# Performance work log

Measured on AMD Instinct MI355X. Metric: run time of the kernel, lower is better.

Reference implementation:

```python
import jax, jax.numpy as jnp
import numpy as np

DIM = 512
NUM_HEADS = 8
NUM_BLOCKS = 16
# NOTE: original code computes head_dim from FULL dim (before the reduce layer),
# so scale = (dim // num_heads) ** -0.5 = 64 ** -0.5, even though the actual
# per-head dim after reduce is 32. We preserve this quirk faithfully.
SCALE = (DIM // NUM_HEADS) ** -0.5


def setup_inputs() -> dict:
    key = jax.random.key(0)
    ks = jax.random.split(key, 5)
    B, N = 4, 4096
    C = DIM // 2
    x = jax.random.normal(ks[0], (B, N, DIM), dtype=jnp.float32)
    reduce_w = jax.random.normal(ks[1], (DIM, C), dtype=jnp.float32) * (DIM ** -0.5)
    qkv_w = jax.random.normal(ks[2], (C, 3 * C), dtype=jnp.float32) * (C ** -0.5)
    proj_w = jax.random.normal(ks[3], (C, DIM), dtype=jnp.float32) * (C ** -0.5)
    proj_b = jnp.zeros((DIM,), dtype=jnp.float32)
    return {"x": x, "reduce_w": reduce_w, "qkv_w": qkv_w,
            "proj_w": proj_w, "proj_b": proj_b}


def reference(x, reduce_w, qkv_w, proj_w, proj_b):
    B, N, _ = x.shape
    xr = x @ reduce_w                      # [B, N, C]  (C = dim/2)
    C = xr.shape[-1]
    H = NUM_HEADS
    d = C // H
    qkv = (xr @ qkv_w).reshape(B, N, 3, H, d).transpose(2, 0, 3, 1, 4)  # [3,B,H,N,d]
    q, k, v = qkv[0], qkv[1], qkv[2]
    bs = N // NUM_BLOCKS                   # block (chunk) size
    # block-diagonal local attention: reshape seq into independent blocks
    qb = q.reshape(B, H, NUM_BLOCKS, bs, d)
    kb = k.reshape(B, H, NUM_BLOCKS, bs, d)
    vb = v.reshape(B, H, NUM_BLOCKS, bs, d)
    attn = jnp.einsum('bhnqd,bhnkd->bhnqk', qb, kb) * SCALE
    attn = jax.nn.softmax(attn, axis=-1)
    ob = jnp.einsum('bhnqk,bhnkd->bhnqd', attn, vb)   # [B,H,Nb,bs,d]
    # torch: per-block transpose(1,2) then cat on dim=1 -> [B, N, H, d]
    o = ob.transpose(0, 2, 3, 1, 4).reshape(B, N, C)
    return o @ proj_w + proj_b
```

## Files before the change

kernel.cpp:

```cpp
#include <hip/hip_runtime.h>
#include <hip/hip_fp16.h>

typedef _Float16 half_t;
typedef _Float16 f16x8 __attribute__((ext_vector_type(8)));
typedef __fp16 fp16x2 __attribute__((ext_vector_type(2)));
typedef float f32x4 __attribute__((ext_vector_type(4)));

#define MFMA_F16(a, b, c) __builtin_amdgcn_mfma_f32_16x16x32_f16((a), (b), (c), 0, 0, 0)

static __device__ inline unsigned pkrtz(float a, float b) {
    union { fp16x2 h; unsigned u; } c;
    c.h = __builtin_amdgcn_cvt_pkrtz(a, b);
    return c.u;
}

__global__ __launch_bounds__(256) void prep(
    const float* __restrict__ qw, const float* __restrict__ rw,
    const float* __restrict__ pw, half_t* __restrict__ pw_t,
    half_t* __restrict__ Wt) {
    __shared__ __align__(16) char smem[24576];
    const int bid = blockIdx.x, tid = threadIdx.x;

    if (bid < 48) {
        char* As = smem;
        char* Bs = smem + 8192;
        const int M0 = (bid % 12) * 64, N0 = (bid / 12) * 128;
        const int lane = tid & 63, w = tid >> 6;
        const int l15 = lane & 15, l4 = lane >> 4;
        const int wrow = (w >> 1) * 32, wcol = (w & 1) * 64;
        const int pa = (l15 & 7) << 4;

        f32x4 acc[2][4];
#pragma unroll
        for (int i = 0; i < 2; ++i)
#pragma unroll
            for (int j = 0; j < 4; ++j) acc[i][j] = (f32x4){0.f, 0.f, 0.f, 0.f};

        for (int kc = 0; kc < 4; ++kc) {
            int c0 = kc * 64;
            __syncthreads();
#pragma unroll
            for (int i = 0; i < 2; ++i) {
                int j = tid + i * 256;
                int row = j >> 3, e8 = (j & 7) * 8;
                float s = (M0 + row) < 256 ? 0.18033688f : 1.f;
                f16x8 v;
#pragma unroll
                for (int e = 0; e < 8; ++e)
                    v[e] = (half_t)(qw[(size_t)(c0 + e8 + e) * 768 + M0 + row] * s);
                *(f16x8*)(As + row * 128 + ((e8 * 2) ^ ((row & 7) << 4))) = v;
            }
#pragma unroll
            for (int i = 0; i < 4; ++i) {
                int j = tid + i * 256;
                int row = j >> 3, e8 = (j & 7) * 8;
                const float* p = rw + (size_t)(N0 + row) * 256 + c0 + e8;
                float4 u0 = *(const float4*)p;
                float4 u1 = *(const float4*)(p + 4);
                f16x8 v;
                v[0] = (half_t)u0.x; v[1] = (half_t)u0.y;
                v[2] = (half_t)u0.z; v[3] = (half_t)u0.w;
                v[4] = (half_t)u1.x; v[5] = (half_t)u1.y;
                v[6] = (half_t)u1.z; v[7] = (half_t)u1.w;
                *(f16x8*)(Bs + row * 128 + ((e8 * 2) ^ ((row & 7) << 4))) = v;
            }
            __syncthreads();
#pragma unroll
            for (int ki = 0; ki < 2; ++ki) {
                f16x8 af[2], bf[4];
#pragma unroll
                for (int mi = 0; mi < 2; ++mi) {
                    int row = wrow + mi * 16 + l15;
                    af[mi] = *(const f16x8*)(As + row * 128 + (((ki * 4 + l4) << 4) ^ pa));
                }
#pragma unroll
                for (int nj = 0; nj < 4; ++nj) {
                    int row = wcol + nj * 16 + l15;
                    bf[nj] = *(const f16x8*)(Bs + row * 128 + (((ki * 4 + l4) << 4) ^ pa));
                }
#pragma unroll
                for (int mi = 0; mi < 2; ++mi)
#pragma unroll
                    for (int nj = 0; nj < 4; ++nj)
                        acc[mi][nj] = MFMA_F16(af[mi], bf[nj], acc[mi][nj]);
            }
        }
#pragma unroll
        for (int mi = 0; mi < 2; ++mi)
#pragma unroll
            for (int nj = 0; nj < 4; ++nj)
#pragma unroll
                for (int reg = 0; reg < 4; ++reg) {
                    int grow = M0 + wrow + mi * 16 + l4 * 4 + reg;
                    int gcol = N0 + wcol + nj * 16 + l15;
                    Wt[(size_t)grow * 512 + gcol] = (half_t)acc[mi][nj][reg];
                }
        return;
    }

    half_t* tile = (half_t*)smem;
    int t = bid - 48;
    int R0 = (t >> 3) * 64, C0 = (t & 7) * 64;
#pragma unroll
    for (int e = 0; e < 16; ++e) {
        int idx = tid + e * 256;
        int r = idx >> 6, c = idx & 63;
        tile[r * 72 + c] = (half_t)pw[(size_t)(R0 + r) * 512 + C0 + c];
    }
    __syncthreads();
#pragma unroll
    for (int e = 0; e < 16; ++e) {
        int idx = tid + e * 256;
        int c = idx >> 6, r = idx & 63;
        pw_t[(size_t)(C0 + c) * 256 + R0 + r] = tile[r * 72 + c];
    }
}

template <int EPI, bool AFP32, int NB, int K>
__global__ __launch_bounds__(256) void gemm_f16(
    const void* __restrict__ Aop, const half_t* __restrict__ Bt,
    void* __restrict__ Dst, const float* __restrict__ bias) {
    constexpr int nkt = K >> 6;
    constexpr int NBC = NB / 32;
    __shared__ __align__(16) char smem[8192 + NB * 128];
    char* As = smem;
    char* Bs = smem + 8192;

    const int tid = threadIdx.x;
    const int lane = tid & 63, w = tid >> 6;
    const int l15 = lane & 15, l4 = lane >> 4;
    const int wrow = (w >> 1) * 32, wcol = (w & 1) * (NB / 2);
    const int bm0 = blockIdx.x * 64;
    const int bn0 = blockIdx.y * NB;
    const int pa = (l15 & 7) << 4;

    f32x4 acc[2][NBC];
#pragma unroll
    for (int i = 0; i < 2; ++i)
#pragma unroll
        for (int j = 0; j < NBC; ++j) acc[i][j] = (f32x4){0.f, 0.f, 0.f, 0.f};

    f16x8 aReg[2], bReg[NBC];

    auto load_tile = [&](int kt) {
#pragma unroll
        for (int i = 0; i < 2; ++i) {
            int c = tid + i * 256;
            int row = c >> 3, k0 = (c & 7) * 8;
            int gk = kt * 64 + k0;
            if (AFP32) {
                const float* Af = (const float*)Aop + (size_t)(bm0 + row) * K + gk;
                float4 u0 = *(const float4*)Af;
                float4 u1 = *(const float4*)(Af + 4);
                f16x8 v;
                v[0] = (half_t)u0.x; v[1] = (half_t)u0.y;
                v[2] = (half_t)u0.z; v[3] = (half_t)u0.w;
                v[4] = (half_t)u1.x; v[5] = (half_t)u1.y;
                v[6] = (half_t)u1.z; v[7] = (half_t)u1.w;
                aReg[i] = v;
            } else {
                aReg[i] = *(const f16x8*)((const half_t*)Aop + (size_t)(bm0 + row) * K + gk);
            }
        }
#pragma unroll
        for (int i = 0; i < NBC; ++i) {
            int c = tid + i * 256;
            int row = c >> 3, k0 = (c & 7) * 8;
            bReg[i] = *(const f16x8*)(Bt + (size_t)(bn0 + row) * K + kt * 64 + k0);
        }
    };

    load_tile(0);
    for (int kt = 0; kt < nkt; ++kt) {
        __syncthreads();
#pragma unroll
        for (int i = 0; i < 2; ++i) {
            int c = tid + i * 256;
            int row = c >> 3, k0 = (c & 7) * 8;
            *(f16x8*)(As + row * 128 + ((k0 * 2) ^ ((row & 7) << 4))) = aReg[i];
        }
#pragma unroll
        for (int i = 0; i < NBC; ++i) {
            int c = tid + i * 256;
            int row = c >> 3, k0 = (c & 7) * 8;
            *(f16x8*)(Bs + row * 128 + ((k0 * 2) ^ ((row & 7) << 4))) = bReg[i];
        }
        __syncthreads();
        if (kt + 1 < nkt) load_tile(kt + 1);
#pragma unroll
        for (int ki = 0; ki < 2; ++ki) {
            f16x8 af[2], bf[NBC];
#pragma unroll
            for (int mi = 0; mi < 2; ++mi) {
                int row = wrow + mi * 16 + l15;
                af[mi] = *(const f16x8*)(As + row * 128 + (((ki * 4 + l4) << 4) ^ pa));
            }
#pragma unroll
            for (int nj = 0; nj < NBC; ++nj) {
                int row = wcol + nj * 16 + l15;
                bf[nj] = *(const f16x8*)(Bs + row * 128 + (((ki * 4 + l4) << 4) ^ pa));
            }
#pragma unroll
            for (int mi = 0; mi < 2; ++mi)
#pragma unroll
                for (int nj = 0; nj < NBC; ++nj)
                    acc[mi][nj] = MFMA_F16(af[mi], bf[nj], acc[mi][nj]);
        }
    }

#pragma unroll
    for (int mi = 0; mi < 2; ++mi) {
#pragma unroll
        for (int nj = 0; nj < NBC; ++nj) {
#pragma unroll
            for (int reg = 0; reg < 4; ++reg) {
                int grow = bm0 + wrow + mi * 16 + l4 * 4 + reg;
                int gcol = bn0 + wcol + nj * 16 + l15;
                float val = acc[mi][nj][reg];
                if (EPI == 1) {
                    int t = gcol >> 8, h = (gcol >> 5) & 7, dd = gcol & 31;
                    int b = grow >> 12, n = grow & 4095;
                    int blk = n >> 8, r = n & 255;
                    size_t base = (size_t)t * 4194304 +
                                  (size_t)((((b << 3) + h) << 4) + blk) * 8192;
                    size_t idx = (t == 2) ? base + (size_t)dd * 256 + r
                                          : base + (size_t)r * 32 + dd;
                    ((half_t*)Dst)[idx] = (half_t)val;
                } else {
                    ((float*)Dst)[(size_t)grow * 512 + gcol] = val + bias[gcol];
                }
            }
        }
    }
}

__global__ __launch_bounds__(512, 4) void attn_f16(const half_t* __restrict__ qkv_ws,
                                                   half_t* __restrict__ o_ws) {
    const int blkid = blockIdx.x;
    const int b = blkid >> 7, h = (blkid >> 4) & 7, blk = blkid & 15;
    const half_t* Q  = qkv_ws + (size_t)blkid * 8192;
    const half_t* Kp = qkv_ws + 4194304 + (size_t)blkid * 8192;
    const half_t* VT = qkv_ws + 8388608 + (size_t)blkid * 8192;

    const int tid = threadIdx.x, lane = tid & 63, w = tid >> 6;
    const int l15 = lane & 15, l4 = lane >> 4;
    const int qb = w * 32;

    f16x8 aq[2];
    aq[0] = *(const f16x8*)(Q + (qb + l15) * 32 + l4 * 8);
    aq[1] = *(const f16x8*)(Q + (qb + 16 + l15) * 32 + l4 * 8);

    float s_run[2] = {0.f, 0.f};
    f32x4 acc_o[2][2];
#pragma unroll
    for (int qg = 0; qg < 2; ++qg)
#pragma unroll
        for (int fo = 0; fo < 2; ++fo) acc_o[qg][fo] = (f32x4){0.f, 0.f, 0.f, 0.f};
    const f32x4 zero4 = (f32x4){0.f, 0.f, 0.f, 0.f};

    for (int kt = 0; kt < 4; ++kt) {
        f16x8 ka[4];
#pragma unroll
        for (int t = 0; t < 4; ++t)
            ka[t] = *(const f16x8*)(Kp + (kt * 64 + t * 16 + l15) * 32 + l4 * 8);
        f16x8 bv[2][2];
#pragma unroll
        for (int c = 0; c < 2; ++c)
#pragma unroll
            for (int fo = 0; fo < 2; ++fo)
                bv[c][fo] = *(const f16x8*)(VT + (fo * 16 + l15) * 256 + kt * 64 + c * 32 + l4 * 8);

        f32x4 st[2][4];
        __builtin_amdgcn_s_setprio(1);
#pragma unroll
        for (int qg = 0; qg < 2; ++qg)
#pragma unroll
            for (int t = 0; t < 4; ++t) st[qg][t] = MFMA_F16(ka[t], aq[qg], zero4);
        __builtin_amdgcn_s_setprio(0);

#pragma unroll
        for (int qg = 0; qg < 2; ++qg) {
            float p[4][4];
            float ps = 0.f;
#pragma unroll
            for (int t = 0; t < 4; ++t)
#pragma unroll
                for (int r = 0; r < 4; ++r) {
                    float e = exp2f(st[qg][t][r]);
                    p[t][r] = e;
                    ps += e;
                }
            ps += __shfl_xor(ps, 16);
            ps += __shfl_xor(ps, 32);
            s_run[qg] += ps;

#pragma unroll
            for (int c = 0; c < 2; ++c) {
                unsigned pk0[2], pk1[2];
#pragma unroll
                for (int rp = 0; rp < 2; ++rp) {
                    pk0[rp] = pkrtz(p[2 * c][2 * rp], p[2 * c][2 * rp + 1]);
                    pk1[rp] = pkrtz(p[2 * c + 1][2 * rp], p[2 * c + 1][2 * rp + 1]);
                }
                union { unsigned u[4]; f16x8 v; } au;
#pragma unroll
                for (int j = 0; j < 4; ++j) {
                    int src = l15 + ((((l4 & 1) << 1) + (j >> 1)) << 4);
                    unsigned g0 = (unsigned)__shfl((int)pk0[j & 1], src);
                    unsigned g1 = (unsigned)__shfl((int)pk1[j & 1], src);
                    au.u[j] = (l4 < 2) ? g0 : g1;
                }
                __builtin_amdgcn_s_setprio(1);
#pragma unroll
                for (int fo = 0; fo < 2; ++fo)
                    acc_o[qg][fo] = MFMA_F16(au.v, bv[c][fo], acc_o[qg][fo]);
                __builtin_amdgcn_s_setprio(0);
            }
        }
    }

#pragma unroll
    for (int qg = 0; qg < 2; ++qg) {
        float inv = 1.f / s_run[qg];
        float sinv[4];
#pragma unroll
        for (int r = 0; r < 4; ++r) sinv[r] = __shfl(inv, (l4 << 2) | r);
#pragma unroll
        for (int fo = 0; fo < 2; ++fo)
#pragma unroll
            for (int r = 0; r < 4; ++r) {
                int grow = b * 4096 + blk * 256 + qb + qg * 16 + l4 * 4 + r;
                o_ws[(size_t)grow * 256 + h * 32 + fo * 16 + l15] =
                    (half_t)(acc_o[qg][fo][r] * sinv[r]);
            }
    }
}

extern "C" void kernel_launch(void* const* d_in, const int* in_sizes, int n_in,
                              void* d_out, int out_size, void* d_ws, size_t ws_size,
                              hipStream_t stream) {
    const float* x        = (const float*)d_in[0];
    const float* reduce_w = (const float*)d_in[1];
    const float* qkv_w    = (const float*)d_in[2];
    const float* proj_w   = (const float*)d_in[3];
    const float* proj_b   = (const float*)d_in[4];
    char* ws = (char*)d_ws;

    half_t* qkv_ws = (half_t*)ws;
    half_t* o_buf  = (half_t*)(ws + 25165824);
    half_t* pw_t   = (half_t*)(ws + 33554432);
    half_t* Wt     = (half_t*)(ws + 33816576);

    prep<<<80, 256, 0, stream>>>(qkv_w, reduce_w, proj_w, pw_t, Wt);
    gemm_f16<1, true, 192, 512><<<dim3(256, 4), 256, 0, stream>>>(x, Wt, qkv_ws, nullptr);
    attn_f16<<<512, 512, 0, stream>>>(qkv_ws, o_buf);
    gemm_f16<2, false, 256, 256><<<dim3(256, 2), 256, 0, stream>>>(o_buf, pw_t, d_out, proj_b);
}
```

Baseline: 71.69 us.

## Fuse QKV projection into attention kernel and widen proj GEMM tiles

Result: faster. 65.04 us (-9.3%).

```diff
diff --git a/kernel.cpp b/kernel.cpp
--- a/kernel.cpp
+++ b/kernel.cpp
@@ -17,7 +17,7 @@
 __global__ __launch_bounds__(256) void prep(
     const float* __restrict__ qw, const float* __restrict__ rw,
     const float* __restrict__ pw, half_t* __restrict__ pw_t,
-    half_t* __restrict__ Wt) {
+    half_t* __restrict__ W3) {
     __shared__ __align__(16) char smem[24576];
     const int bid = blockIdx.x, tid = threadIdx.x;
 
@@ -91,9 +91,11 @@
             for (int nj = 0; nj < 4; ++nj)
 #pragma unroll
                 for (int reg = 0; reg < 4; ++reg) {
-                    int grow = M0 + wrow + mi * 16 + l4 * 4 + reg;
+                    int n = M0 + wrow + mi * 16 + l4 * 4 + reg;
                     int gcol = N0 + wcol + nj * 16 + l15;
-                    Wt[(size_t)grow * 512 + gcol] = (half_t)acc[mi][nj][reg];
+                    int part = n >> 8, hh = (n & 255) >> 5, dd = n & 31;
+                    W3[(size_t)(hh * 96 + part * 32 + dd) * 512 + gcol] =
+                        (half_t)acc[mi][nj][reg];
                 }
         return;
     }
@@ -116,139 +118,115 @@
     }
 }
 
-template <int EPI, bool AFP32, int NB, int K>
-__global__ __launch_bounds__(256) void gemm_f16(
-    const void* __restrict__ Aop, const half_t* __restrict__ Bt,
-    void* __restrict__ Dst, const float* __restrict__ bias) {
-    constexpr int nkt = K >> 6;
-    constexpr int NBC = NB / 32;
-    __shared__ __align__(16) char smem[8192 + NB * 128];
+__global__ __launch_bounds__(512, 4) void qkv_attn(
+    const float* __restrict__ X, const half_t* __restrict__ W3,
+    half_t* __restrict__ o_ws) {
+    __shared__ __align__(16) char smem[50176];
     char* As = smem;
-    char* Bs = smem + 8192;
-
-    const int tid = threadIdx.x;
-    const int lane = tid & 63, w = tid >> 6;
-    const int l15 = lane & 15, l4 = lane >> 4;
-    const int wrow = (w >> 1) * 32, wcol = (w & 1) * (NB / 2);
-    const int bm0 = blockIdx.x * 64;
-    const int bn0 = blockIdx.y * NB;
-    const int pa = (l15 & 7) << 4;
-
-    f32x4 acc[2][NBC];
-#pragma unroll
-    for (int i = 0; i < 2; ++i)
-#pragma unroll
-        for (int j = 0; j < NBC; ++j) acc[i][j] = (f32x4){0.f, 0.f, 0.f, 0.f};
-
-    f16x8 aReg[2], bReg[NBC];
-
-    auto load_tile = [&](int kt) {
-#pragma unroll
-        for (int i = 0; i < 2; ++i) {
-            int c = tid + i * 256;
-            int row = c >> 3, k0 = (c & 7) * 8;
-            int gk = kt * 64 + k0;
-            if (AFP32) {
-                const float* Af = (const float*)Aop + (size_t)(bm0 + row) * K + gk;
-                float4 u0 = *(const float4*)Af;
-                float4 u1 = *(const float4*)(Af + 4);
-                f16x8 v;
-                v[0] = (half_t)u0.x; v[1] = (half_t)u0.y;
-                v[2] = (half_t)u0.z; v[3] = (half_t)u0.w;
-                v[4] = (half_t)u1.x; v[5] = (half_t)u1.y;
-                v[6] = (half_t)u1.z; v[7] = (half_t)u1.w;
-                aReg[i] = v;
-            } else {
-                aReg[i] = *(const f16x8*)((const half_t*)Aop + (size_t)(bm0 + row) * K + gk);
-            }
-        }
-#pragma unroll
-        for (int i = 0; i < NBC; ++i) {
-            int c = tid + i * 256;
-            int row = c >> 3, k0 = (c & 7) * 8;
-            bReg[i] = *(const f16x8*)(Bt + (size_t)(bn0 + row) * K + kt * 64 + k0);
-        }
-    };
-
-    load_tile(0);
-    for (int kt = 0; kt < nkt; ++kt) {
-        __syncthreads();
-#pragma unroll
-        for (int i = 0; i < 2; ++i) {
-            int c = tid + i * 256;
-            int row = c >> 3, k0 = (c & 7) * 8;
-            *(f16x8*)(As + row * 128 + ((k0 * 2) ^ ((row & 7) << 4))) = aReg[i];
-        }
-#pragma unroll
-        for (int i = 0; i < NBC; ++i) {
-            int c = tid + i * 256;
-            int row = c >> 3, k0 = (c & 7) * 8;
-            *(f16x8*)(Bs + row * 128 + ((k0 * 2) ^ ((row & 7) << 4))) = bReg[i];
-        }
-        __syncthreads();
-        if (kt + 1 < nkt) load_tile(kt + 1);
-#pragma unroll
-        for (int ki = 0; ki < 2; ++ki) {
-            f16x8 af[2], bf[NBC];
-#pragma unroll
-            for (int mi = 0; mi < 2; ++mi) {
-                int row = wrow + mi * 16 + l15;
-                af[mi] = *(const f16x8*)(As + row * 128 + (((ki * 4 + l4) << 4) ^ pa));
-            }
-#pragma unroll
-            for (int nj = 0; nj < NBC; ++nj) {
-                int row = wcol + nj * 16 + l15;
-                bf[nj] = *(const f16x8*)(Bs + row * 128 + (((ki * 4 + l4) << 4) ^ pa));
-            }
-#pragma unroll
-            for (int mi = 0; mi < 2; ++mi)
-#pragma unroll
-                for (int nj = 0; nj < NBC; ++nj)
-                    acc[mi][nj] = MFMA_F16(af[mi], bf[nj], acc[mi][nj]);
-        }
-    }
-
-#pragma unroll
-    for (int mi = 0; mi < 2; ++mi) {
-#pragma unroll
-        for (int nj = 0; nj < NBC; ++nj) {
-#pragma unroll
-            for (int reg = 0; reg < 4; ++reg) {
-                int grow = bm0 + wrow + mi * 16 + l4 * 4 + reg;
-                int gcol = bn0 + wcol + nj * 16 + l15;
-                float val = acc[mi][nj][reg];
-                if (EPI == 1) {
-                    int t = gcol >> 8, h = (gcol >> 5) & 7, dd = gcol & 31;
-                    int b = grow >> 12, n = grow & 4095;
-                    int blk = n >> 8, r = n & 255;
-                    size_t base = (size_t)t * 4194304 +
-                                  (size_t)((((b << 3) + h) << 4) + blk) * 8192;
-                    size_t idx = (t == 2) ? base + (size_t)dd * 256 + r
-                                          : base + (size_t)r * 32 + dd;
-                    ((half_t*)Dst)[idx] = (half_t)val;
-                } else {
-                    ((float*)Dst)[(size_t)grow * 512 + gcol] = val + bias[gcol];
-                }
-            }
-        }
-    }
-}
-
-__global__ __launch_bounds__(512, 4) void attn_f16(const half_t* __restrict__ qkv_ws,
-                                                   half_t* __restrict__ o_ws) {
-    const int blkid = blockIdx.x;
-    const int b = blkid >> 7, h = (blkid >> 4) & 7, blk = blkid & 15;
-    const half_t* Q  = qkv_ws + (size_t)blkid * 8192;
-    const half_t* Kp = qkv_ws + 4194304 + (size_t)blkid * 8192;
-    const half_t* VT = qkv_ws + 8388608 + (size_t)blkid * 8192;
-
+    char* Bs = smem + 32768;
+    half_t* q_lds = (half_t*)smem;
+    half_t* k_lds = (half_t*)(smem + 16384);
+    half_t* vT    = (half_t*)(smem + 32768);
+
+    const int bid = blockIdx.x;
+    const int h = bid >> 6, gb = bid & 63, b = gb >> 4, blk = gb & 15;
     const int tid = threadIdx.x, lane = tid & 63, w = tid >> 6;
     const int l15 = lane & 15, l4 = lane >> 4;
+    const int pa = (l15 & 7) << 4;
+
+    const float* Xt = X + (size_t)(b * 4096 + blk * 256) * 512;
+    const half_t* Bh = W3 + (size_t)h * 96 * 512;
+
+    f32x4 acc[2][6];
+#pragma unroll
+    for (int i = 0; i < 2; ++i)
+#pragma unroll
+        for (int j = 0; j < 6; ++j) acc[i][j] = (f32x4){0.f, 0.f, 0.f, 0.f};
+
+    f16x8 aReg[4], bReg[2];
+
+    auto load_tile = [&](int kt) {
+#pragma unroll
+        for (int i = 0; i < 4; ++i) {
+            int J = tid + i * 512;
+            int row = J >> 3, c = (J & 7) ^ (row & 7);
+            const float* p = Xt + (size_t)row * 512 + kt * 64 + c * 8;
+            float4 u0 = *(const float4*)p;
+            float4 u1 = *(const float4*)(p + 4);
+            f16x8 v;
+            v[0] = (half_t)u0.x; v[1] = (half_t)u0.y;
+            v[2] = (half_t)u0.z; v[3] = (half_t)u0.w;
+            v[4] = (half_t)u1.x; v[5] = (half_t)u1.y;
+            v[6] = (half_t)u1.z; v[7] = (half_t)u1.w;
+            aReg[i] = v;
+        }
+        {
+            int J = tid;
+            int row = J >> 3, c = (J & 7) ^ (row & 7);
+            bReg[0] = *(const f16x8*)(Bh + (size_t)row * 512 + kt * 64 + c * 8);
+        }
+        if (tid < 256) {
+            int J = 512 + tid;
+            int row = J >> 3, c = (J & 7) ^ (row & 7);
+            bReg[1] = *(const f16x8*)(Bh + (size_t)row * 512 + kt * 64 + c * 8);
+        }
+    };
+
+    load_tile(0);
+    for (int kt = 0; kt < 8; ++kt) {
+        __syncthreads();
+#pragma unroll
+        for (int i = 0; i < 4; ++i) {
+            int J = tid + i * 512;
+            *(f16x8*)(As + J * 16) = aReg[i];
+        }
+        *(f16x8*)(Bs + tid * 16) = bReg[0];
+        if (tid < 256) *(f16x8*)(Bs + (512 + tid) * 16) = bReg[1];
+        __syncthreads();
+        if (kt + 1 < 8) load_tile(kt + 1);
+#pragma unroll
+        for (int ki = 0; ki < 2; ++ki) {
+            f16x8 af[2], bf[6];
+#pragma unroll
+            for (int mi = 0; mi < 2; ++mi) {
+                int row = w * 32 + mi * 16 + l15;
+                af[mi] = *(const f16x8*)(As + row * 128 + (((ki * 4 + l4) << 4) ^ pa));
+            }
+#pragma unroll
+            for (int nj = 0; nj < 6; ++nj) {
+                int row = nj * 16 + l15;
+                bf[nj] = *(const f16x8*)(Bs + row * 128 + (((ki * 4 + l4) << 4) ^ pa));
+            }
+#pragma unroll
+            for (int mi = 0; mi < 2; ++mi)
+#pragma unroll
+                for (int nj = 0; nj < 6; ++nj)
+                    acc[mi][nj] = MFMA_F16(af[mi], bf[nj], acc[mi][nj]);
+        }
+    }
+
+    __syncthreads();
+#pragma unroll
+    for (int mi = 0; mi < 2; ++mi) {
+#pragma unroll
+        for (int nj = 0; nj < 6; ++nj) {
+#pragma unroll
+            for (int reg = 0; reg < 4; ++reg) {
+                int row = w * 32 + mi * 16 + l4 * 4 + reg;
+                int col = nj * 16 + l15;
+                half_t hv = (half_t)acc[mi][nj][reg];
+                if (col < 32) q_lds[row * 32 + col] = hv;
+                else if (col < 64) k_lds[row * 32 + (col - 32)] = hv;
+                else vT[(col - 64) * 264 + row] = hv;
+            }
+        }
+    }
+    __syncthreads();
+
     const int qb = w * 32;
-
     f16x8 aq[2];
-    aq[0] = *(const f16x8*)(Q + (qb + l15) * 32 + l4 * 8);
-    aq[1] = *(const f16x8*)(Q + (qb + 16 + l15) * 32 + l4 * 8);
+    aq[0] = *(const f16x8*)&q_lds[(qb + l15) * 32 + l4 * 8];
+    aq[1] = *(const f16x8*)&q_lds[(qb + 16 + l15) * 32 + l4 * 8];
 
     float s_run[2] = {0.f, 0.f};
     f32x4 acc_o[2][2];
@@ -262,13 +240,13 @@
         f16x8 ka[4];
 #pragma unroll
         for (int t = 0; t < 4; ++t)
-            ka[t] = *(const f16x8*)(Kp + (kt * 64 + t * 16 + l15) * 32 + l4 * 8);
+            ka[t] = *(const f16x8*)&k_lds[(kt * 64 + t * 16 + l15) * 32 + l4 * 8];
         f16x8 bv[2][2];
 #pragma unroll
         for (int c = 0; c < 2; ++c)
 #pragma unroll
             for (int fo = 0; fo < 2; ++fo)
-                bv[c][fo] = *(const f16x8*)(VT + (fo * 16 + l15) * 256 + kt * 64 + c * 32 + l4 * 8);
+                bv[c][fo] = *(const f16x8*)&vT[(fo * 16 + l15) * 264 + kt * 64 + c * 32 + l4 * 8];
 
         f32x4 st[2][4];
         __builtin_amdgcn_s_setprio(1);
@@ -334,6 +312,92 @@
                     (half_t)(acc_o[qg][fo][r] * sinv[r]);
             }
     }
+}
+
+__global__ __launch_bounds__(512) void gemm_proj(
+    const half_t* __restrict__ A, const half_t* __restrict__ Bt,
+    float* __restrict__ Dst, const float* __restrict__ bias) {
+    __shared__ __align__(16) char smem[16384 + 32768];
+    char* As = smem;
+    char* Bs = smem + 16384;
+
+    const int tid = threadIdx.x;
+    const int lane = tid & 63, w = tid >> 6;
+    const int l15 = lane & 15, l4 = lane >> 4;
+    const int wrow = (w >> 1) * 32, wcol = (w & 1) * 128;
+    const int bm0 = blockIdx.x * 128;
+    const int bn0 = blockIdx.y * 256;
+    const int pa = (l15 & 7) << 4;
+
+    f32x4 acc[2][8];
+#pragma unroll
+    for (int i = 0; i < 2; ++i)
+#pragma unroll
+        for (int j = 0; j < 8; ++j) acc[i][j] = (f32x4){0.f, 0.f, 0.f, 0.f};
+
+    f16x8 aReg[2], bReg[4];
+
+    auto load_tile = [&](int kt) {
+#pragma unroll
+        for (int i = 0; i < 2; ++i) {
+            int J = tid + i * 512;
+            int row = J >> 3, c = (J & 7) ^ (row & 7);
+            aReg[i] = *(const f16x8*)(A + (size_t)(bm0 + row) * 256 + kt * 64 + c * 8);
+        }
+#pragma unroll
+        for (int i = 0; i < 4; ++i) {
+            int J = tid + i * 512;
+            int row = J >> 3, c = (J & 7) ^ (row & 7);
+            bReg[i] = *(const f16x8*)(Bt + (size_t)(bn0 + row) * 256 + kt * 64 + c * 8);
+        }
+    };
+
+    load_tile(0);
+    for (int kt = 0; kt < 4; ++kt) {
+        __syncthreads();
+#pragma unroll
+        for (int i = 0; i < 2; ++i) {
+            int J = tid + i * 512;
+            *(f16x8*)(As + J * 16) = aReg[i];
+        }
+#pragma unroll
+        for (int i = 0; i < 4; ++i) {
+            int J = tid + i * 512;
+            *(f16x8*)(Bs + J * 16) = bReg[i];
+        }
+        __syncthreads();
+        if (kt + 1 < 4) load_tile(kt + 1);
+#pragma unroll
+        for (int ki = 0; ki < 2; ++ki) {
+            f16x8 af[2], bf[8];
+#pragma unroll
+            for (int mi = 0; mi < 2; ++mi) {
+                int row = wrow + mi * 16 + l15;
+                af[mi] = *(const f16x8*)(As + row * 128 + (((ki * 4 + l4) << 4) ^ pa));
+            }
+#pragma unroll
+            for (int nj = 0; nj < 8; ++nj) {
+                int row = wcol + nj * 16 + l15;
+                bf[nj] = *(const f16x8*)(Bs + row * 128 + (((ki * 4 + l4) << 4) ^ pa));
+            }
+#pragma unroll
+            for (int mi = 0; mi < 2; ++mi)
+#pragma unroll
+                for (int nj = 0; nj < 8; ++nj)
+                    acc[mi][nj] = MFMA_F16(af[mi], bf[nj], acc[mi][nj]);
+        }
+    }
+
+#pragma unroll
+    for (int mi = 0; mi < 2; ++mi)
+#pragma unroll
+        for (int nj = 0; nj < 8; ++nj)
+#pragma unroll
+            for (int reg = 0; reg < 4; ++reg) {
+                int grow = bm0 + wrow + mi * 16 + l4 * 4 + reg;
+                int gcol = bn0 + wcol + nj * 16 + l15;
+                Dst[(size_t)grow * 512 + gcol] = acc[mi][nj][reg] + bias[gcol];
+            }
 }
 
 extern "C" void kernel_launch(void* const* d_in, const int* in_sizes, int n_in,
@@ -346,13 +410,11 @@
     const float* proj_b   = (const float*)d_in[4];
     char* ws = (char*)d_ws;
 
-    half_t* qkv_ws = (half_t*)ws;
-    half_t* o_buf  = (half_t*)(ws + 25165824);
-    half_t* pw_t   = (half_t*)(ws + 33554432);
-    half_t* Wt     = (half_t*)(ws + 33816576);
-
-    prep<<<80, 256, 0, stream>>>(qkv_w, reduce_w, proj_w, pw_t, Wt);
-    gemm_f16<1, true, 192, 512><<<dim3(256, 4), 256, 0, stream>>>(x, Wt, qkv_ws, nullptr);
-    attn_f16<<<512, 512, 0, stream>>>(qkv_ws, o_buf);
-    gemm_f16<2, false, 256, 256><<<dim3(256, 2), 256, 0, stream>>>(o_buf, pw_t, d_out, proj_b);
+    half_t* o_buf = (half_t*)ws;
+    half_t* pw_t  = (half_t*)(ws + 8388608);
+    half_t* W3    = (half_t*)(ws + 8650752);
+
+    prep<<<80, 256, 0, stream>>>(qkv_w, reduce_w, proj_w, pw_t, W3);
+    qkv_attn<<<512, 512, 0, stream>>>(x, W3, o_buf);
+    gemm_proj<<<dim3(128, 2), 512, 0, stream>>>(o_buf, pw_t, (float*)d_out, proj_b);
 }
```
